# Optimization experiments

Hardware: AMD Instinct MI355X
Metric: run time of the kernel (lower is better)

Reference implementation:

```python
import jax, jax.numpy as jnp
import numpy as np

B, C, H, E, K, QT = 256, 1024, 64, 64, 2, 20000

def _mlp(x, W1, b1, W2, b2):
    # GKT MLP (eval mode: dropout off; batch-norm omitted, see notes)
    return jax.nn.relu(jax.nn.relu(x @ W1 + b1) @ W2 + b2)

def setup_inputs() -> dict:
    key = jax.random.key(0)
    ks = jax.random.split(key, 30)
    s = 0.05  # weight scale to keep pre-clamp activations in a sane range
    xt = jax.random.uniform(ks[0], (B,), dtype=jnp.float32)
    qt = jax.random.randint(ks[1], (B,), 0, QT)
    ht = jax.random.normal(ks[2], (B, C, H), dtype=jnp.float32)
    # binary question->concept incidence, ~4 KCs per question, col 0 forced on
    oh = (jax.random.uniform(ks[3], (QT, C)) < 4.0 / C).astype(jnp.float32)
    oh = oh.at[:, 0].set(1.0)
    qt_kc_one_hot = jnp.concatenate([oh, jnp.zeros((1, C), jnp.float32)], axis=0)  # zero padding row
    kc_embeddings = jax.random.normal(ks[4], (C, E), dtype=jnp.float32) * 0.1
    graphs = jax.random.uniform(ks[5], (K, C, C), dtype=jnp.float32)  # graph_model output
    neigh_weight = jnp.float32(0.8)
    MI = H + E
    Ws1 = jax.random.normal(ks[6], (MI, H), jnp.float32) * s; bs1 = jnp.zeros((H,), jnp.float32)
    Ws2 = jax.random.normal(ks[7], (H, H), jnp.float32) * s;  bs2 = jnp.zeros((H,), jnp.float32)
    Wn1 = jax.random.normal(ks[8], (K, 2 * MI, H), jnp.float32) * s; bn1 = jnp.zeros((K, H), jnp.float32)
    Wn2 = jax.random.normal(ks[9], (K, H, H), jnp.float32) * s;      bn2 = jnp.zeros((K, H), jnp.float32)
    ea_w = jax.random.uniform(ks[10], (C,), dtype=jnp.float32)
    We = jax.random.normal(ks[11], (H, H), jnp.float32) * s; be = jnp.zeros((H,), jnp.float32)
    Wa = jax.random.normal(ks[12], (H, H), jnp.float32) * s; ba = jnp.zeros((H,), jnp.float32)
    W_ih = jax.random.normal(ks[13], (H, 3 * H), jnp.float32) * s; b_ih = jnp.zeros((3 * H,), jnp.float32)
    W_hh = jax.random.normal(ks[14], (H, 3 * H), jnp.float32) * s; b_hh = jnp.zeros((3 * H,), jnp.float32)
    Wp = jax.random.normal(ks[15], (H, 1), jnp.float32) * s; bp = jnp.zeros((1,), jnp.float32)
    return dict(xt=xt, qt=qt, ht=ht, qt_kc_one_hot=qt_kc_one_hot, kc_embeddings=kc_embeddings,
                graphs=graphs, neigh_weight=neigh_weight, Ws1=Ws1, bs1=bs1, Ws2=Ws2, bs2=bs2,
                Wn1=Wn1, bn1=bn1, Wn2=Wn2, bn2=bn2, ea_w=ea_w, We=We, be=be, Wa=Wa, ba=ba,
                W_ih=W_ih, b_ih=b_ih, W_hh=W_hh, b_hh=b_hh, Wp=Wp, bp=bp)

def reference(xt, qt, ht, qt_kc_one_hot, kc_embeddings, graphs, neigh_weight,
              Ws1, bs1, Ws2, bs2, Wn1, bn1, Wn2, bn2, ea_w, We, be, Wa, ba,
              W_ih, b_ih, W_hh, b_hh, Wp, bp):
    # ---- _aggregate: the fusion loops never write back, so tmp_ht = cat(ht, kc_emb)
    mask = qt_kc_one_hot[qt]                                   # [B, C] gather of binary incidence
    kc = jnp.broadcast_to(kc_embeddings[None], (mask.shape[0], C, E))
    tmp_ht = jnp.concatenate([ht, kc], axis=-1)                # [B, C, H+E]
    # ---- _agg_neighbors
    self_ht = tmp_ht * mask[..., None]
    self_feat = jnp.clip(_mlp(self_ht, Ws1, bs1, Ws2, bs2), -10.0, 10.0)
    neigh_ht = jnp.clip(jnp.concatenate([self_ht, tmp_ht], axis=-1), -5.0, 5.0)  # [B,C,2(H+E)]
    # bug-faithful adj: mean of graphs[k] rows over sample 0's active concepts
    a0 = mask[0]                                               # [C]
    denom = jnp.maximum(a0.sum(), 1.0)
    adj = jnp.clip(jnp.einsum('c,kcd->kd', a0, graphs) / denom, -5.0, 5.0)       # [K, C]
    nb = jax.vmap(lambda W1, b1, W2, b2: _mlp(neigh_ht, W1, b1, W2, b2))(Wn1, bn1, Wn2, bn2)
    nb = jnp.clip(nb, -5.0, 5.0)                               # [K, B, C, H]
    w = jnp.clip(neigh_weight, 0.1, 0.9)
    nf = jnp.clip(adj[0][None, :, None] * nb[0], -5.0, 5.0)
    for k in range(1, K):
        nf = jnp.clip(w * nf + (1.0 - w) * adj[k][None, :, None] * nb[k], -5.0, 5.0)
    m_next = jnp.clip(jnp.where(mask[..., None] > 0.5, self_feat, nf), -50.0, 50.0)
    # ---- erase-add gate
    g = ea_w[None, :, None]
    res = m_next - g * jax.nn.sigmoid(m_next @ We + be) * m_next + g * jnp.tanh(m_next @ Wa + ba)
    # ---- GRUCell over flattened (B*C) rows
    gi = res @ W_ih + b_ih
    gh = ht @ W_hh + b_hh
    ir, iz, in_ = jnp.split(gi, 3, axis=-1)
    hr, hz, hn = jnp.split(gh, 3, axis=-1)
    r = jax.nn.sigmoid(ir + hr)
    z = jax.nn.sigmoid(iz + hz)
    n = jnp.tanh(in_ + r * hn)
    h_next = (1.0 - z) * n + z * ht                            # [B, C, H]
    y = jax.nn.sigmoid(h_next @ Wp + bp)[..., 0]               # [B, C]
    return y
```

## Files before the change

### kernel.cpp

```cpp
#include <hip/hip_runtime.h>

#define DEVINL __device__ __forceinline__

typedef __bf16 bf16x8 __attribute__((ext_vector_type(8)));
typedef float  f32x4  __attribute__((ext_vector_type(4)));
typedef unsigned u32x2 __attribute__((ext_vector_type(2)));

static constexpr size_t kAdjOff  = 0;
static constexpr size_t kBiasOff = 8192;
static constexpr size_t kFragOff = 8192 + 786432;

static constexpr int FB_Wn1h0 = 0,  FB_Wn1h1 = 8,  FB_Wn2_0 = 16, FB_Wn2_1 = 24;
static constexpr int FB_Ws1h  = 32, FB_Ws2   = 40, FB_We    = 48, FB_Wa    = 56;
static constexpr int FB_Wih   = 64, FB_Whh   = 88;

DEVINL unsigned short bf16r(float f) {
  unsigned u = __builtin_bit_cast(unsigned, f);
  unsigned r = ((u >> 16) & 1u) + 0x7FFFu;
  return (unsigned short)((u + r) >> 16);
}
DEVINL float sigmoidf_(float x) { return __builtin_amdgcn_rcpf(1.f + __expf(-x)); }
DEVINL float tanhf_(float x)    { return 1.f - 2.f * __builtin_amdgcn_rcpf(1.f + __expf(2.f * x)); }

DEVINL unsigned pkbf(float a, float b) {
  unsigned d;
  asm("v_cvt_pk_bf16_f32 %0, %1, %2" : "=v"(d) : "v"(a), "v"(b));
  return d;
}

DEVINL f32x4 mfma16(bf16x8 a, bf16x8 b, f32x4 c) {
  return __builtin_amdgcn_mfma_f32_16x16x32_bf16(a, b, c, 0, 0, 0);
}

DEVINL unsigned clip2_(unsigned x) {
  float lo = __builtin_bit_cast(float, x << 16);
  float hi = __builtin_bit_cast(float, x & 0xFFFF0000u);
  lo = fminf(fmaxf(lo, -5.f), 5.f);
  hi = fminf(fmaxf(hi, -5.f), 5.f);
  return (__builtin_bit_cast(unsigned, lo) >> 16) | (__builtin_bit_cast(unsigned, hi) & 0xFFFF0000u);
}
DEVINL bf16x8 clip5(bf16x8 a) {
  uint4 u = __builtin_bit_cast(uint4, a);
  u.x = clip2_(u.x); u.y = clip2_(u.y); u.z = clip2_(u.z); u.w = clip2_(u.w);
  return __builtin_bit_cast(bf16x8, u);
}

DEVINL void dsw64(unsigned addr, unsigned long long d) {
  asm volatile("ds_write_b64 %0, %1" :: "v"(addr), "v"(d));
}
DEVINL void ldA2_tr(unsigned addr, bf16x8& a0, bf16x8& a1) {
  u32x2 r0, r1, r2, r3;
  asm volatile(
      "ds_read_b64_tr_b16 %0, %4\n\t"
      "ds_read_b64_tr_b16 %1, %4 offset:512\n\t"
      "ds_read_b64_tr_b16 %2, %4 offset:1024\n\t"
      "ds_read_b64_tr_b16 %3, %4 offset:1536\n\t"
      "s_waitcnt lgkmcnt(0)"
      : "=&v"(r0), "=&v"(r1), "=&v"(r2), "=&v"(r3)
      : "v"(addr));
  uint4 u0{r0.x, r0.y, r1.x, r1.y};
  uint4 u1{r2.x, r2.y, r3.x, r3.y};
  a0 = __builtin_bit_cast(bf16x8, u0);
  a1 = __builtin_bit_cast(bf16x8, u1);
}

__global__ void prep_adj_kernel(const int* __restrict__ qt, const float* __restrict__ onehot,
                                const float* __restrict__ graphs, float* __restrict__ adjw) {
  __shared__ float a0v[1024];
  __shared__ int   aidx[1024];
  __shared__ int   s_nnz;
  __shared__ float s_den;
  const int tid = threadIdx.x;
  const int k = blockIdx.x >> 2, chunk = blockIdx.x & 3;
  if (tid == 0) { s_nnz = 0; s_den = 0.f; }
  __syncthreads();
  const int q0 = qt[0];
  float lsum = 0.f;
#pragma unroll
  for (int i = 0; i < 4; i++) {
    int c = tid * 4 + i;
    float v = onehot[(size_t)q0 * 1024 + c];
    lsum += v;
    if (v != 0.f) { int p = atomicAdd(&s_nnz, 1); aidx[p] = c; a0v[p] = v; }
  }
#pragma unroll
  for (int off = 32; off >= 1; off >>= 1) lsum += __shfl_xor(lsum, off, 64);
  if ((tid & 63) == 0) atomicAdd(&s_den, lsum);
  __syncthreads();
  const float denom = fmaxf(s_den, 1.f);
  const int nnz = s_nnz;
  const int d = chunk * 256 + tid;
  const float* G = graphs + (size_t)k * 1048576 + d;
  float sum = 0.f;
  for (int j = 0; j < nnz; j++) sum += a0v[j] * G[(size_t)aidx[j] * 1024];
  adjw[k * 1024 + d] = fminf(fmaxf(sum / denom, -5.f), 5.f);
}

__global__ void prep_bias_kernel(const float* __restrict__ kc, const float* __restrict__ Wn1,
                                 const float* __restrict__ bn1, const float* __restrict__ Ws1,
                                 const float* __restrict__ bs1, float* __restrict__ biasTab) {
  int gid = blockIdx.x * 256 + threadIdx.x;
  int j = gid & 63;
  int c = (gid >> 6) & 1023;
  int tab = gid >> 16;
  const float* kcr = kc + (size_t)c * 64;
  float s;
  if (tab < 2) {
    s = bn1[tab * 64 + j];
    const float* W = Wn1 + ((size_t)tab * 256 + 192) * 64 + j;
#pragma unroll 4
    for (int e = 0; e < 64; e++) s += fminf(fmaxf(kcr[e], -5.f), 5.f) * W[(size_t)e * 64];
  } else {
    s = bs1[j];
    const float* W = Ws1 + (size_t)64 * 64 + j;
#pragma unroll 4
    for (int e = 0; e < 64; e++) s += kcr[e] * W[(size_t)e * 64];
  }
  int c16 = c >> 4, rr = c & 3, qq = (c & 15) >> 2, nt = j >> 4;
  int lane = qq * 16 + (j & 15);
  biasTab[(size_t)((((c16 * 3 + tab) * 4 + nt) * 64 + lane)) * 4 + rr] = s;
}

__global__ void prep_wfrag_kernel(const float* __restrict__ Wn1, const float* __restrict__ Wn2,
                                  const float* __restrict__ Ws1, const float* __restrict__ Ws2,
                                  const float* __restrict__ We,  const float* __restrict__ Wa,
                                  const float* __restrict__ Wih, const float* __restrict__ Whh,
                                  uint4* __restrict__ wfrag) {
  const int bid = blockIdx.x, lane = threadIdx.x;
  int mat, ks, nt;
  if (bid < 64) { mat = bid >> 3; ks = (bid >> 2) & 1; nt = bid & 3; }
  else { int f2 = bid - 64; mat = 8 + f2 / 24; int f = f2 % 24; ks = f / 12; nt = f % 12; }
  const float* base = Wn1; int stride = 64;
  switch (mat) {
    case 0: base = Wn1 + (size_t)128 * 64; break;
    case 1: base = Wn1 + (size_t)(256 + 128) * 64; break;
    case 2: base = Wn2; break;
    case 3: base = Wn2 + (size_t)64 * 64; break;
    case 4: base = Ws1; break;
    case 5: base = Ws2; break;
    case 6: base = We; break;
    case 7: base = Wa; break;
    case 8: base = Wih; stride = 192; break;
    case 9: base = Whh; stride = 192; break;
  }
  const int qq = lane >> 4, col = nt * 16 + (lane & 15);
  union { unsigned short u[8]; uint4 v; } tmp;
#pragma unroll
  for (int jj = 0; jj < 8; jj++) {
    int k = ks * 32 + ((jj < 4) ? (qq * 4 + jj) : (16 + qq * 4 + (jj - 4)));
    tmp.u[jj] = bf16r(base[(size_t)k * stride + col]);
  }
  wfrag[(size_t)bid * 64 + lane] = tmp.v;
}

__global__ __launch_bounds__(256, 3) void gkt_main_kernel(
    const int* __restrict__ qt, const float* __restrict__ onehot, const float* __restrict__ ht,
    const float* __restrict__ nw, const float* __restrict__ bn2, const float* __restrict__ be,
    const float* __restrict__ ba, const float* __restrict__ bih, const float* __restrict__ bhh,
    const float* __restrict__ Wp, const float* __restrict__ bp, const float* __restrict__ eaw,
    const float* __restrict__ bs2, const float* __restrict__ adjw, const float* __restrict__ biasTab,
    const bf16x8* __restrict__ wfrag, float* __restrict__ out) {
  __shared__ __align__(128) unsigned short hbuf[4][64][16];
  __shared__ __align__(16) float tokp[4][64];
  __shared__ __align__(16) uint4 gfrag[40 * 64];

  const int tid = threadIdx.x;
  const int wv = tid >> 6, lane = tid & 63;
  const int q = lane >> 4, cl = lane & 15;
  const int t0 = (blockIdx.x * 4 + wv) * 16;
  const int b = t0 >> 10, c0 = t0 & 1023, c16 = c0 >> 4;

  unsigned short* hb = &hbuf[wv][0][0];
  float* tp = &tokp[wv][0];
  const unsigned hbA = (unsigned)(size_t)hb + lane * 8;

  {
    const uint4* wf4 = (const uint4*)wfrag;
#pragma unroll
    for (int i = 0; i < 10; i++) {
      int f = wv * 10 + i;
      gfrag[f * 64 + lane] = wf4[(64 + f) * 64 + lane];
    }
  }

  if (lane < 16) {
    const int c = c0 + lane;
    tp[lane]      = onehot[(size_t)qt[b] * 1024 + c];
    tp[16 + lane] = adjw[c];
    tp[32 + lane] = adjw[1024 + c];
    tp[48 + lane] = eaw[c];
  }
  {
    const float4* ht4 = (const float4*)ht;
#pragma unroll
    for (int i = 0; i < 4; i++) {
      float4 v = ht4[(size_t)t0 * 16 + i * 64 + lane];
      int e = i * 64 + lane;
      int tok = e >> 4, fb = (e & 15) * 4;
      hbuf[wv][fb + 0][tok] = bf16r(v.x);
      hbuf[wv][fb + 1][tok] = bf16r(v.y);
      hbuf[wv][fb + 2][tok] = bf16r(v.z);
      hbuf[wv][fb + 3][tok] = bf16r(v.w);
    }
  }

  const f32x4* bt4 = (const f32x4*)biasTab;
  f32x4 btN0[4], btN1[4], btS[4];
#pragma unroll
  for (int nt = 0; nt < 4; nt++) {
    btN0[nt] = bt4[((c16 * 3 + 0) * 4 + nt) * 64 + lane];
    btN1[nt] = bt4[((c16 * 3 + 1) * 4 + nt) * 64 + lane];
    btS[nt]  = bt4[((c16 * 3 + 2) * 4 + nt) * 64 + lane];
  }

  __syncthreads();

  const float wmix = fminf(fmaxf(nw[0], 0.1f), 0.9f);

  auto ldB = [&](int frag) -> bf16x8 { return wfrag[frag * 64 + lane]; };
  auto ldG = [&](int fr) -> bf16x8 {
    return (fr < 40) ? *(const bf16x8*)&gfrag[fr * 64 + lane]
                     : wfrag[(64 + fr) * 64 + lane];
  };
  auto ldTP4 = [&](int base) -> f32x4 {
    return *(const f32x4*)(tp + base + q * 4);
  };
  auto packRow = [&](int nt, float v0, float v1, float v2, float v3) {
    unsigned long long d = (unsigned long long)pkbf(v0, v1) |
                           ((unsigned long long)pkbf(v2, v3) << 32);
    dsw64((unsigned)(size_t)&hbuf[wv][nt * 16 + cl][q * 4], d);
  };

  bf16x8 xr[2];
  ldA2_tr(hbA, xr[0], xr[1]);

  f32x4 nf[4];
  {
    bf16x8 xc[2];
#pragma unroll
    for (int ks = 0; ks < 2; ks++) xc[ks] = clip5(xr[ks]);

#pragma unroll
    for (int k2 = 0; k2 < 2; k2++) {
      f32x4 acc[4];
#pragma unroll
      for (int nt = 0; nt < 4; nt++)
        acc[nt] = k2 ? btN1[nt] : btN0[nt];
#pragma unroll
      for (int ks = 0; ks < 2; ks++)
#pragma unroll
        for (int nt = 0; nt < 4; nt++) {
          bf16x8 bb = ldB((k2 ? FB_Wn1h1 : FB_Wn1h0) + ks * 4 + nt);
          acc[nt] = mfma16(xc[ks], bb, acc[nt]);
        }
#pragma unroll
      for (int nt = 0; nt < 4; nt++)
        packRow(nt, fmaxf(acc[nt][0], 0.f), fmaxf(acc[nt][1], 0.f),
                    fmaxf(acc[nt][2], 0.f), fmaxf(acc[nt][3], 0.f));
      bf16x8 a0, a1;
      ldA2_tr(hbA, a0, a1);
      f32x4 acc2[4];
#pragma unroll
      for (int nt = 0; nt < 4; nt++) {
        float bz = bn2[k2 * 64 + nt * 16 + cl];
        acc2[nt] = {bz, bz, bz, bz};
      }
#pragma unroll
      for (int nt = 0; nt < 4; nt++) {
        acc2[nt] = mfma16(a0, ldB((k2 ? FB_Wn2_1 : FB_Wn2_0) + nt), acc2[nt]);
        acc2[nt] = mfma16(a1, ldB((k2 ? FB_Wn2_1 : FB_Wn2_0) + 4 + nt), acc2[nt]);
      }
      {
        f32x4 adjv = ldTP4((1 + k2) * 16);
#pragma unroll
        for (int nt = 0; nt < 4; nt++)
#pragma unroll
          for (int r = 0; r < 4; r++) {
            float nb = fminf(fmaxf(acc2[nt][r], 0.f), 5.f);
            float v = adjv[r] * nb;
            if (k2 == 0) nf[nt][r] = wmix * fminf(fmaxf(v, -5.f), 5.f);
            else         nf[nt][r] = fminf(fmaxf(nf[nt][r] + (1.f - wmix) * v, -5.f), 5.f);
          }
      }
    }
  }

  bool anySelf = __any((lane < 16) && (tp[lane] > 0.5f));
  if (anySelf) {
    f32x4 acc[4];
#pragma unroll
    for (int nt = 0; nt < 4; nt++) acc[nt] = btS[nt];
#pragma unroll
    for (int ks = 0; ks < 2; ks++)
#pragma unroll
      for (int nt = 0; nt < 4; nt++) {
        bf16x8 bb = ldB(FB_Ws1h + ks * 4 + nt);
        acc[nt] = mfma16(xr[ks], bb, acc[nt]);
      }
#pragma unroll
    for (int nt = 0; nt < 4; nt++)
      packRow(nt, fmaxf(acc[nt][0], 0.f), fmaxf(acc[nt][1], 0.f),
                  fmaxf(acc[nt][2], 0.f), fmaxf(acc[nt][3], 0.f));
    bf16x8 a0, a1;
    ldA2_tr(hbA, a0, a1);
    f32x4 acc2[4];
#pragma unroll
    for (int nt = 0; nt < 4; nt++) {
      float bz = bs2[nt * 16 + cl];
      acc2[nt] = {bz, bz, bz, bz};
    }
#pragma unroll
    for (int nt = 0; nt < 4; nt++) {
      acc2[nt] = mfma16(a0, ldB(FB_Ws2 + nt), acc2[nt]);
      acc2[nt] = mfma16(a1, ldB(FB_Ws2 + 4 + nt), acc2[nt]);
    }
    {
      f32x4 mk = ldTP4(0);
#pragma unroll
      for (int nt = 0; nt < 4; nt++)
#pragma unroll
        for (int r = 0; r < 4; r++) {
          float sf = fminf(fmaxf(acc2[nt][r], 0.f), 10.f);
          nf[nt][r] = (mk[r] > 0.5f) ? sf : nf[nt][r];
        }
    }
  }

#pragma unroll
  for (int nt = 0; nt < 4; nt++)
    packRow(nt, nf[nt][0], nf[nt][1], nf[nt][2], nf[nt][3]);
  bf16x8 mf[2];
  ldA2_tr(hbA, mf[0], mf[1]);
  {
    f32x4 accE[4];
#pragma unroll
    for (int nt = 0; nt < 4; nt++) {
      float bz = be[nt * 16 + cl];
      accE[nt] = {bz, bz, bz, bz};
    }
#pragma unroll
    for (int ks = 0; ks < 2; ks++)
#pragma unroll
      for (int nt = 0; nt < 4; nt++) {
        bf16x8 bb = ldB(FB_We + ks * 4 + nt);
        accE[nt] = mfma16(mf[ks], bb, accE[nt]);
      }
    {
      f32x4 gv = ldTP4(48);
#pragma unroll
      for (int nt = 0; nt < 4; nt++)
#pragma unroll
        for (int r = 0; r < 4; r++) {
          float m = nf[nt][r];
          nf[nt][r] = m - gv[r] * sigmoidf_(accE[nt][r]) * m;
        }
    }
    f32x4 accA[4];
#pragma unroll
    for (int nt = 0; nt < 4; nt++) {
      float bz = ba[nt * 16 + cl];
      accA[nt] = {bz, bz, bz, bz};
    }
#pragma unroll
    for (int ks = 0; ks < 2; ks++)
#pragma unroll
      for (int nt = 0; nt < 4; nt++) {
        bf16x8 bb = ldB(FB_Wa + ks * 4 + nt);
        accA[nt] = mfma16(mf[ks], bb, accA[nt]);
      }
    {
      f32x4 gv = ldTP4(48);
#pragma unroll
      for (int nt = 0; nt < 4; nt++)
#pragma unroll
        for (int r = 0; r < 4; r++)
          nf[nt][r] += gv[r] * tanhf_(accA[nt][r]);
    }
  }

#pragma unroll
  for (int nt = 0; nt < 4; nt++)
    packRow(nt, nf[nt][0], nf[nt][1], nf[nt][2], nf[nt][3]);
  bf16x8 rf[2];
  ldA2_tr(hbA, rf[0], rf[1]);

  f32x4 gR[4], gZ[4], gN[4], gH[4];
#pragma unroll
  for (int nt = 0; nt < 4; nt++) {
    int col = nt * 16 + cl;
    float brz = bih[col] + bhh[col];
    float bzz = bih[64 + col] + bhh[64 + col];
    float bnn = bih[128 + col];
    float bhn = bhh[128 + col];
    gR[nt] = {brz, brz, brz, brz};
    gZ[nt] = {bzz, bzz, bzz, bzz};
    gN[nt] = {bnn, bnn, bnn, bnn};
    gH[nt] = {bhn, bhn, bhn, bhn};
  }
#pragma unroll
  for (int ks = 0; ks < 2; ks++)
#pragma unroll
    for (int nt = 0; nt < 4; nt++) {
      bf16x8 bi_r = ldG(ks * 12 + nt);
      bf16x8 bh_r = ldG(24 + ks * 12 + nt);
      bf16x8 bi_z = ldG(ks * 12 + 4 + nt);
      bf16x8 bh_z = ldG(24 + ks * 12 + 4 + nt);
      bf16x8 bi_n = ldG(ks * 12 + 8 + nt);
      bf16x8 bh_n = ldG(24 + ks * 12 + 8 + nt);
      gR[nt] = mfma16(rf[ks], bi_r, gR[nt]);
      gR[nt] = mfma16(xr[ks], bh_r, gR[nt]);
      gZ[nt] = mfma16(rf[ks], bi_z, gZ[nt]);
      gZ[nt] = mfma16(xr[ks], bh_z, gZ[nt]);
      gN[nt] = mfma16(rf[ks], bi_n, gN[nt]);
      gH[nt] = mfma16(xr[ks], bh_n, gH[nt]);
    }

  float wp4[4];
#pragma unroll
  for (int nt = 0; nt < 4; nt++) wp4[nt] = Wp[nt * 16 + cl];
  const float bpv = bp[0];

#pragma unroll
  for (int r = 0; r < 4; r++) {
    int tok = q * 4 + r;
    float part = 0.f;
#pragma unroll
    for (int nt = 0; nt < 4; nt++) {
      float rr = sigmoidf_(gR[nt][r]);
      float zz = sigmoidf_(gZ[nt][r]);
      float nval = tanhf_(gN[nt][r] + rr * gH[nt][r]);
      float htv = ht[(size_t)(t0 + tok) * 64 + nt * 16 + cl];
      float hnx = (1.f - zz) * nval + zz * htv;
      part += hnx * wp4[nt];
    }
    part += __shfl_xor(part, 1, 64);
    part += __shfl_xor(part, 2, 64);
    part += __shfl_xor(part, 4, 64);
    part += __shfl_xor(part, 8, 64);
    if (cl == 0) out[t0 + tok] = sigmoidf_(part + bpv);
  }
}

extern "C" void kernel_launch(void* const* d_in, const int* in_sizes, int n_in,
                              void* d_out, int out_size, void* d_ws, size_t ws_size,
                              hipStream_t stream) {
  const int*   qt     = (const int*)d_in[1];
  const float* ht     = (const float*)d_in[2];
  const float* onehot = (const float*)d_in[3];
  const float* kc     = (const float*)d_in[4];
  const float* graphs = (const float*)d_in[5];
  const float* nw     = (const float*)d_in[6];
  const float* Ws1    = (const float*)d_in[7];
  const float* bs1    = (const float*)d_in[8];
  const float* Ws2    = (const float*)d_in[9];
  const float* bs2    = (const float*)d_in[10];
  const float* Wn1    = (const float*)d_in[11];
  const float* bn1    = (const float*)d_in[12];
  const float* Wn2    = (const float*)d_in[13];
  const float* bn2    = (const float*)d_in[14];
  const float* eaw    = (const float*)d_in[15];
  const float* We     = (const float*)d_in[16];
  const float* be     = (const float*)d_in[17];
  const float* Wa     = (const float*)d_in[18];
  const float* ba     = (const float*)d_in[19];
  const float* Wih    = (const float*)d_in[20];
  const float* bih    = (const float*)d_in[21];
  const float* Whh    = (const float*)d_in[22];
  const float* bhh    = (const float*)d_in[23];
  const float* Wp     = (const float*)d_in[24];
  const float* bp     = (const float*)d_in[25];
  float* out = (float*)d_out;

  float* adjw    = (float*)((char*)d_ws + kAdjOff);
  float* biasTab = (float*)((char*)d_ws + kBiasOff);
  uint4* wfragU  = (uint4*)((char*)d_ws + kFragOff);

  prep_adj_kernel<<<8, 256, 0, stream>>>(qt, onehot, graphs, adjw);
  prep_bias_kernel<<<768, 256, 0, stream>>>(kc, Wn1, bn1, Ws1, bs1, biasTab);
  prep_wfrag_kernel<<<112, 64, 0, stream>>>(Wn1, Wn2, Ws1, Ws2, We, Wa, Wih, Whh, wfragU);
  gkt_main_kernel<<<4096, 256, 0, stream>>>(qt, onehot, ht, nw, bn2, be, ba, bih, bhh,
                                            Wp, bp, eaw, bs2, adjw, biasTab,
                                            (const bf16x8*)wfragU, out);
}
```

Baseline: 276.0 us.

## Process two 16-token tiles per wave to reuse weight fragments in registers

Each wave now handles 32 tokens as two 16-token sub-tiles (A/B) that share weight fragments loaded once into registers (fX/fY), rather than reloading them from global memory for every MFMA. The grid is halved and launch bounds drop from 3 to 2 blocks per SIMD to leave room for the larger register footprint. The aim is to cut repeated global and L2 weight-fragment traffic and give more independent MFMAs to interleave. The cost is lower occupancy and higher register pressure, which may limit latency hiding.

Result: faster. 266.6 us (-3.4%).

```diff
diff --git a/kernel.cpp b/kernel.cpp
--- a/kernel.cpp
+++ b/kernel.cpp
@@ -153,26 +153,29 @@
   wfrag[(size_t)bid * 64 + lane] = tmp.v;
 }
 
-__global__ __launch_bounds__(256, 3) void gkt_main_kernel(
+__global__ __launch_bounds__(256, 2) void gkt_main_kernel(
     const int* __restrict__ qt, const float* __restrict__ onehot, const float* __restrict__ ht,
     const float* __restrict__ nw, const float* __restrict__ bn2, const float* __restrict__ be,
     const float* __restrict__ ba, const float* __restrict__ bih, const float* __restrict__ bhh,
     const float* __restrict__ Wp, const float* __restrict__ bp, const float* __restrict__ eaw,
     const float* __restrict__ bs2, const float* __restrict__ adjw, const float* __restrict__ biasTab,
     const bf16x8* __restrict__ wfrag, float* __restrict__ out) {
-  __shared__ __align__(128) unsigned short hbuf[4][64][16];
-  __shared__ __align__(16) float tokp[4][64];
+  __shared__ __align__(128) unsigned short hbuf[4][2][64][16];
+  __shared__ __align__(16) float tokp[4][2][64];
   __shared__ __align__(16) uint4 gfrag[40 * 64];
 
   const int tid = threadIdx.x;
   const int wv = tid >> 6, lane = tid & 63;
   const int q = lane >> 4, cl = lane & 15;
-  const int t0 = (blockIdx.x * 4 + wv) * 16;
+  const int t0 = (blockIdx.x * 4 + wv) * 32;
   const int b = t0 >> 10, c0 = t0 & 1023, c16 = c0 >> 4;
 
-  unsigned short* hb = &hbuf[wv][0][0];
-  float* tp = &tokp[wv][0];
-  const unsigned hbA = (unsigned)(size_t)hb + lane * 8;
+  const unsigned hbA = (unsigned)(size_t)&hbuf[wv][0][0][0] + lane * 8;
+  const unsigned hbB = hbA + 2048;
+  const unsigned pbA = (unsigned)(size_t)&hbuf[wv][0][0][0] + cl * 32 + q * 8;
+  const unsigned pbB = pbA + 2048;
+  float* tpA = &tokp[wv][0][0];
+  float* tpB = &tokp[wv][1][0];
 
   {
     const uint4* wf4 = (const uint4*)wfrag;
@@ -183,208 +186,261 @@
     }
   }
 
-  if (lane < 16) {
+  if (lane < 32) {
+    const int s = lane >> 4, l = lane & 15;
     const int c = c0 + lane;
-    tp[lane]      = onehot[(size_t)qt[b] * 1024 + c];
-    tp[16 + lane] = adjw[c];
-    tp[32 + lane] = adjw[1024 + c];
-    tp[48 + lane] = eaw[c];
+    float* tp = &tokp[wv][s][0];
+    tp[l]      = onehot[(size_t)qt[b] * 1024 + c];
+    tp[16 + l] = adjw[c];
+    tp[32 + l] = adjw[1024 + c];
+    tp[48 + l] = eaw[c];
   }
   {
     const float4* ht4 = (const float4*)ht;
 #pragma unroll
-    for (int i = 0; i < 4; i++) {
+    for (int i = 0; i < 8; i++) {
       float4 v = ht4[(size_t)t0 * 16 + i * 64 + lane];
       int e = i * 64 + lane;
-      int tok = e >> 4, fb = (e & 15) * 4;
-      hbuf[wv][fb + 0][tok] = bf16r(v.x);
-      hbuf[wv][fb + 1][tok] = bf16r(v.y);
-      hbuf[wv][fb + 2][tok] = bf16r(v.z);
-      hbuf[wv][fb + 3][tok] = bf16r(v.w);
-    }
-  }
-
-  const f32x4* bt4 = (const f32x4*)biasTab;
-  f32x4 btN0[4], btN1[4], btS[4];
-#pragma unroll
-  for (int nt = 0; nt < 4; nt++) {
-    btN0[nt] = bt4[((c16 * 3 + 0) * 4 + nt) * 64 + lane];
-    btN1[nt] = bt4[((c16 * 3 + 1) * 4 + nt) * 64 + lane];
-    btS[nt]  = bt4[((c16 * 3 + 2) * 4 + nt) * 64 + lane];
-  }
-
-  __syncthreads();
-
-  const float wmix = fminf(fmaxf(nw[0], 0.1f), 0.9f);
+      int tok = e >> 4, s = tok >> 4, tk = tok & 15, fb = (e & 15) * 4;
+      hbuf[wv][s][fb + 0][tk] = bf16r(v.x);
+      hbuf[wv][s][fb + 1][tk] = bf16r(v.y);
+      hbuf[wv][s][fb + 2][tk] = bf16r(v.z);
+      hbuf[wv][s][fb + 3][tk] = bf16r(v.w);
+    }
+  }
 
   auto ldB = [&](int frag) -> bf16x8 { return wfrag[frag * 64 + lane]; };
   auto ldG = [&](int fr) -> bf16x8 {
     return (fr < 40) ? *(const bf16x8*)&gfrag[fr * 64 + lane]
                      : wfrag[(64 + fr) * 64 + lane];
   };
-  auto ldTP4 = [&](int base) -> f32x4 {
+  auto ldTP4 = [&](const float* tp, int base) -> f32x4 {
     return *(const f32x4*)(tp + base + q * 4);
   };
-  auto packRow = [&](int nt, float v0, float v1, float v2, float v3) {
+  auto packRow = [&](unsigned pb, int nt, float v0, float v1, float v2, float v3) {
     unsigned long long d = (unsigned long long)pkbf(v0, v1) |
                            ((unsigned long long)pkbf(v2, v3) << 32);
-    dsw64((unsigned)(size_t)&hbuf[wv][nt * 16 + cl][q * 4], d);
+    dsw64(pb + nt * 512, d);
   };
-
-  bf16x8 xr[2];
-  ldA2_tr(hbA, xr[0], xr[1]);
-
-  f32x4 nf[4];
+  const f32x4* bt4 = (const f32x4*)biasTab;
+
+  bf16x8 fX[8], fY[8];
+#pragma unroll
+  for (int i = 0; i < 8; i++) fX[i] = ldB(FB_Wn1h0 + i);
+
+  __syncthreads();
+
+  const float wmix = fminf(fmaxf(nw[0], 0.1f), 0.9f);
+
+  bf16x8 xrA[2], xrB[2];
+  ldA2_tr(hbA, xrA[0], xrA[1]);
+  ldA2_tr(hbB, xrB[0], xrB[1]);
+  bf16x8 xcA[2], xcB[2];
+#pragma unroll
+  for (int ks = 0; ks < 2; ks++) { xcA[ks] = clip5(xrA[ks]); xcB[ks] = clip5(xrB[ks]); }
+
+  f32x4 nfA[4], nfB[4];
+
+#pragma unroll
+  for (int k2 = 0; k2 < 2; k2++) {
+#pragma unroll
+    for (int i = 0; i < 8; i++) fY[i] = ldB((k2 ? FB_Wn2_1 : FB_Wn2_0) + i);
+    f32x4 acA[4], acB[4];
+#pragma unroll
+    for (int nt = 0; nt < 4; nt++) {
+      acA[nt] = bt4[((c16 * 3 + k2) * 4 + nt) * 64 + lane];
+      acB[nt] = bt4[(((c16 + 1) * 3 + k2) * 4 + nt) * 64 + lane];
+    }
+#pragma unroll
+    for (int ks = 0; ks < 2; ks++)
+#pragma unroll
+      for (int nt = 0; nt < 4; nt++) {
+        acA[nt] = mfma16(xcA[ks], fX[ks * 4 + nt], acA[nt]);
+        acB[nt] = mfma16(xcB[ks], fX[ks * 4 + nt], acB[nt]);
+      }
+#pragma unroll
+    for (int nt = 0; nt < 4; nt++)
+      packRow(pbA, nt, fmaxf(acA[nt][0], 0.f), fmaxf(acA[nt][1], 0.f),
+                       fmaxf(acA[nt][2], 0.f), fmaxf(acA[nt][3], 0.f));
+#pragma unroll
+    for (int nt = 0; nt < 4; nt++)
+      packRow(pbB, nt, fmaxf(acB[nt][0], 0.f), fmaxf(acB[nt][1], 0.f),
+                       fmaxf(acB[nt][2], 0.f), fmaxf(acB[nt][3], 0.f));
+
+#pragma unroll
+    for (int i = 0; i < 8; i++) fX[i] = ldB((k2 ? FB_Ws1h : FB_Wn1h1) + i);
+    bf16x8 a0, a1;
+    f32x4 c2A[4], c2B[4];
+#pragma unroll
+    for (int nt = 0; nt < 4; nt++) {
+      float bz = bn2[k2 * 64 + nt * 16 + cl];
+      c2A[nt] = {bz, bz, bz, bz};
+      c2B[nt] = c2A[nt];
+    }
+    ldA2_tr(hbA, a0, a1);
+#pragma unroll
+    for (int nt = 0; nt < 4; nt++) {
+      c2A[nt] = mfma16(a0, fY[nt], c2A[nt]);
+      c2A[nt] = mfma16(a1, fY[4 + nt], c2A[nt]);
+    }
+    ldA2_tr(hbB, a0, a1);
+#pragma unroll
+    for (int nt = 0; nt < 4; nt++) {
+      c2B[nt] = mfma16(a0, fY[nt], c2B[nt]);
+      c2B[nt] = mfma16(a1, fY[4 + nt], c2B[nt]);
+    }
+    {
+      f32x4 avA = ldTP4(tpA, (1 + k2) * 16), avB = ldTP4(tpB, (1 + k2) * 16);
+#pragma unroll
+      for (int nt = 0; nt < 4; nt++)
+#pragma unroll
+        for (int r = 0; r < 4; r++) {
+          float nbA = fminf(fmaxf(c2A[nt][r], 0.f), 5.f);
+          float nbB = fminf(fmaxf(c2B[nt][r], 0.f), 5.f);
+          float vA = avA[r] * nbA, vB = avB[r] * nbB;
+          if (k2 == 0) {
+            nfA[nt][r] = wmix * fminf(fmaxf(vA, -5.f), 5.f);
+            nfB[nt][r] = wmix * fminf(fmaxf(vB, -5.f), 5.f);
+          } else {
+            nfA[nt][r] = fminf(fmaxf(nfA[nt][r] + (1.f - wmix) * vA, -5.f), 5.f);
+            nfB[nt][r] = fminf(fmaxf(nfB[nt][r] + (1.f - wmix) * vB, -5.f), 5.f);
+          }
+        }
+    }
+  }
+
+  bool anySelf = __any((lane < 32) && (tokp[wv][lane >> 4][lane & 15] > 0.5f));
+  if (anySelf) {
+#pragma unroll
+    for (int i = 0; i < 8; i++) fY[i] = ldB(FB_Ws2 + i);
+    f32x4 acA[4], acB[4];
+#pragma unroll
+    for (int nt = 0; nt < 4; nt++) {
+      acA[nt] = bt4[((c16 * 3 + 2) * 4 + nt) * 64 + lane];
+      acB[nt] = bt4[(((c16 + 1) * 3 + 2) * 4 + nt) * 64 + lane];
+    }
+#pragma unroll
+    for (int ks = 0; ks < 2; ks++)
+#pragma unroll
+      for (int nt = 0; nt < 4; nt++) {
+        acA[nt] = mfma16(xrA[ks], fX[ks * 4 + nt], acA[nt]);
+        acB[nt] = mfma16(xrB[ks], fX[ks * 4 + nt], acB[nt]);
+      }
+#pragma unroll
+    for (int nt = 0; nt < 4; nt++)
+      packRow(pbA, nt, fmaxf(acA[nt][0], 0.f), fmaxf(acA[nt][1], 0.f),
+                       fmaxf(acA[nt][2], 0.f), fmaxf(acA[nt][3], 0.f));
+#pragma unroll
+    for (int nt = 0; nt < 4; nt++)
+      packRow(pbB, nt, fmaxf(acB[nt][0], 0.f), fmaxf(acB[nt][1], 0.f),
+                       fmaxf(acB[nt][2], 0.f), fmaxf(acB[nt][3], 0.f));
+    bf16x8 a0, a1;
+    f32x4 c2A[4], c2B[4];
+#pragma unroll
+    for (int nt = 0; nt < 4; nt++) {
+      float bz = bs2[nt * 16 + cl];
+      c2A[nt] = {bz, bz, bz, bz};
+      c2B[nt] = c2A[nt];
+    }
+    ldA2_tr(hbA, a0, a1);
+#pragma unroll
+    for (int nt = 0; nt < 4; nt++) {
+      c2A[nt] = mfma16(a0, fY[nt], c2A[nt]);
+      c2A[nt] = mfma16(a1, fY[4 + nt], c2A[nt]);
+    }
+    ldA2_tr(hbB, a0, a1);
+#pragma unroll
+    for (int nt = 0; nt < 4; nt++) {
+      c2B[nt] = mfma16(a0, fY[nt], c2B[nt]);
+      c2B[nt] = mfma16(a1, fY[4 + nt], c2B[nt]);
+    }
+    {
+      f32x4 mkA = ldTP4(tpA, 0), mkB = ldTP4(tpB, 0);
+#pragma unroll
+      for (int nt = 0; nt < 4; nt++)
+#pragma unroll
+        for (int r = 0; r < 4; r++) {
+          float sfA = fminf(fmaxf(c2A[nt][r], 0.f), 10.f);
+          float sfB = fminf(fmaxf(c2B[nt][r], 0.f), 10.f);
+          nfA[nt][r] = (mkA[r] > 0.5f) ? sfA : nfA[nt][r];
+          nfB[nt][r] = (mkB[r] > 0.5f) ? sfB : nfB[nt][r];
+        }
+    }
+  }
+
+#pragma unroll
+  for (int i = 0; i < 8; i++) fX[i] = ldB(FB_We + i);
+#pragma unroll
+  for (int nt = 0; nt < 4; nt++) packRow(pbA, nt, nfA[nt][0], nfA[nt][1], nfA[nt][2], nfA[nt][3]);
+#pragma unroll
+  for (int nt = 0; nt < 4; nt++) packRow(pbB, nt, nfB[nt][0], nfB[nt][1], nfB[nt][2], nfB[nt][3]);
+  bf16x8 mfA[2], mfB[2];
+  ldA2_tr(hbA, mfA[0], mfA[1]);
+  ldA2_tr(hbB, mfB[0], mfB[1]);
   {
-    bf16x8 xc[2];
-#pragma unroll
-    for (int ks = 0; ks < 2; ks++) xc[ks] = clip5(xr[ks]);
-
-#pragma unroll
-    for (int k2 = 0; k2 < 2; k2++) {
-      f32x4 acc[4];
-#pragma unroll
-      for (int nt = 0; nt < 4; nt++)
-        acc[nt] = k2 ? btN1[nt] : btN0[nt];
-#pragma unroll
-      for (int ks = 0; ks < 2; ks++)
-#pragma unroll
-        for (int nt = 0; nt < 4; nt++) {
-          bf16x8 bb = ldB((k2 ? FB_Wn1h1 : FB_Wn1h0) + ks * 4 + nt);
-          acc[nt] = mfma16(xc[ks], bb, acc[nt]);
-        }
-#pragma unroll
-      for (int nt = 0; nt < 4; nt++)
-        packRow(nt, fmaxf(acc[nt][0], 0.f), fmaxf(acc[nt][1], 0.f),
-                    fmaxf(acc[nt][2], 0.f), fmaxf(acc[nt][3], 0.f));
-      bf16x8 a0, a1;
-      ldA2_tr(hbA, a0, a1);
-      f32x4 acc2[4];
+#pragma unroll
+    for (int i = 0; i < 8; i++) fY[i] = ldB(FB_Wa + i);
+    f32x4 eA[4], eB[4];
+#pragma unroll
+    for (int nt = 0; nt < 4; nt++) {
+      float bz = be[nt * 16 + cl];
+      eA[nt] = {bz, bz, bz, bz};
+      eB[nt] = eA[nt];
+    }
+#pragma unroll
+    for (int ks = 0; ks < 2; ks++)
 #pragma unroll
       for (int nt = 0; nt < 4; nt++) {
-        float bz = bn2[k2 * 64 + nt * 16 + cl];
-        acc2[nt] = {bz, bz, bz, bz};
-      }
-#pragma unroll
-      for (int nt = 0; nt < 4; nt++) {
-        acc2[nt] = mfma16(a0, ldB((k2 ? FB_Wn2_1 : FB_Wn2_0) + nt), acc2[nt]);
-        acc2[nt] = mfma16(a1, ldB((k2 ? FB_Wn2_1 : FB_Wn2_0) + 4 + nt), acc2[nt]);
-      }
-      {
-        f32x4 adjv = ldTP4((1 + k2) * 16);
-#pragma unroll
-        for (int nt = 0; nt < 4; nt++)
-#pragma unroll
-          for (int r = 0; r < 4; r++) {
-            float nb = fminf(fmaxf(acc2[nt][r], 0.f), 5.f);
-            float v = adjv[r] * nb;
-            if (k2 == 0) nf[nt][r] = wmix * fminf(fmaxf(v, -5.f), 5.f);
-            else         nf[nt][r] = fminf(fmaxf(nf[nt][r] + (1.f - wmix) * v, -5.f), 5.f);
-          }
-      }
-    }
-  }
-
-  bool anySelf = __any((lane < 16) && (tp[lane] > 0.5f));
-  if (anySelf) {
-    f32x4 acc[4];
-#pragma unroll
-    for (int nt = 0; nt < 4; nt++) acc[nt] = btS[nt];
-#pragma unroll
-    for (int ks = 0; ks < 2; ks++)
-#pragma unroll
-      for (int nt = 0; nt < 4; nt++) {
-        bf16x8 bb = ldB(FB_Ws1h + ks * 4 + nt);
-        acc[nt] = mfma16(xr[ks], bb, acc[nt]);
-      }
-#pragma unroll
-    for (int nt = 0; nt < 4; nt++)
-      packRow(nt, fmaxf(acc[nt][0], 0.f), fmaxf(acc[nt][1], 0.f),
-                  fmaxf(acc[nt][2], 0.f), fmaxf(acc[nt][3], 0.f));
-    bf16x8 a0, a1;
-    ldA2_tr(hbA, a0, a1);
-    f32x4 acc2[4];
-#pragma unroll
-    for (int nt = 0; nt < 4; nt++) {
-      float bz = bs2[nt * 16 + cl];
-      acc2[nt] = {bz, bz, bz, bz};
-    }
-#pragma unroll
-    for (int nt = 0; nt < 4; nt++) {
-      acc2[nt] = mfma16(a0, ldB(FB_Ws2 + nt), acc2[nt]);
-      acc2[nt] = mfma16(a1, ldB(FB_Ws2 + 4 + nt), acc2[nt]);
-    }
-    {
-      f32x4 mk = ldTP4(0);
-#pragma unroll
-      for (int nt = 0; nt < 4; nt++)
-#pragma unroll
-        for (int r = 0; r < 4; r++) {
-          float sf = fminf(fmaxf(acc2[nt][r], 0.f), 10.f);
-          nf[nt][r] = (mk[r] > 0.5f) ? sf : nf[nt][r];
-        }
-    }
-  }
-
-#pragma unroll
-  for (int nt = 0; nt < 4; nt++)
-    packRow(nt, nf[nt][0], nf[nt][1], nf[nt][2], nf[nt][3]);
-  bf16x8 mf[2];
-  ldA2_tr(hbA, mf[0], mf[1]);
-  {
-    f32x4 accE[4];
-#pragma unroll
-    for (int nt = 0; nt < 4; nt++) {
-      float bz = be[nt * 16 + cl];
-      accE[nt] = {bz, bz, bz, bz};
-    }
-#pragma unroll
-    for (int ks = 0; ks < 2; ks++)
-#pragma unroll
-      for (int nt = 0; nt < 4; nt++) {
-        bf16x8 bb = ldB(FB_We + ks * 4 + nt);
-        accE[nt] = mfma16(mf[ks], bb, accE[nt]);
+        eA[nt] = mfma16(mfA[ks], fX[ks * 4 + nt], eA[nt]);
+        eB[nt] = mfma16(mfB[ks], fX[ks * 4 + nt], eB[nt]);
       }
     {
-      f32x4 gv = ldTP4(48);
+      f32x4 gvA = ldTP4(tpA, 48), gvB = ldTP4(tpB, 48);
 #pragma unroll
       for (int nt = 0; nt < 4; nt++)
 #pragma unroll
         for (int r = 0; r < 4; r++) {
-          float m = nf[nt][r];
-          nf[nt][r] = m - gv[r] * sigmoidf_(accE[nt][r]) * m;
+          float mA = nfA[nt][r], mB = nfB[nt][r];
+          nfA[nt][r] = mA - gvA[r] * sigmoidf_(eA[nt][r]) * mA;
+          nfB[nt][r] = mB - gvB[r] * sigmoidf_(eB[nt][r]) * mB;
         }
     }
-    f32x4 accA[4];
+    f32x4 aA[4], aB[4];
 #pragma unroll
     for (int nt = 0; nt < 4; nt++) {
       float bz = ba[nt * 16 + cl];
-      accA[nt] = {bz, bz, bz, bz};
+      aA[nt] = {bz, bz, bz, bz};
+      aB[nt] = aA[nt];
     }
 #pragma unroll
     for (int ks = 0; ks < 2; ks++)
 #pragma unroll
       for (int nt = 0; nt < 4; nt++) {
-        bf16x8 bb = ldB(FB_Wa + ks * 4 + nt);
-        accA[nt] = mfma16(mf[ks], bb, accA[nt]);
+        aA[nt] = mfma16(mfA[ks], fY[ks * 4 + nt], aA[nt]);
+        aB[nt] = mfma16(mfB[ks], fY[ks * 4 + nt], aB[nt]);
       }
     {
-      f32x4 gv = ldTP4(48);
+      f32x4 gvA = ldTP4(tpA, 48), gvB = ldTP4(tpB, 48);
 #pragma unroll
       for (int nt = 0; nt < 4; nt++)
 #pragma unroll
-        for (int r = 0; r < 4; r++)
-          nf[nt][r] += gv[r] * tanhf_(accA[nt][r]);
-    }
-  }
-
-#pragma unroll
-  for (int nt = 0; nt < 4; nt++)
-    packRow(nt, nf[nt][0], nf[nt][1], nf[nt][2], nf[nt][3]);
-  bf16x8 rf[2];
-  ldA2_tr(hbA, rf[0], rf[1]);
-
-  f32x4 gR[4], gZ[4], gN[4], gH[4];
+        for (int r = 0; r < 4; r++) {
+          nfA[nt][r] += gvA[r] * tanhf_(aA[nt][r]);
+          nfB[nt][r] += gvB[r] * tanhf_(aB[nt][r]);
+        }
+    }
+  }
+
+#pragma unroll
+  for (int nt = 0; nt < 4; nt++) packRow(pbA, nt, nfA[nt][0], nfA[nt][1], nfA[nt][2], nfA[nt][3]);
+#pragma unroll
+  for (int nt = 0; nt < 4; nt++) packRow(pbB, nt, nfB[nt][0], nfB[nt][1], nfB[nt][2], nfB[nt][3]);
+  bf16x8 rfA[2], rfB[2];
+  ldA2_tr(hbA, rfA[0], rfA[1]);
+  ldA2_tr(hbB, rfB[0], rfB[1]);
+
+  f32x4 gRA[4], gZA[4], gNA[4], gHA[4];
+  f32x4 gRB[4], gZB[4], gNB[4], gHB[4];
 #pragma unroll
   for (int nt = 0; nt < 4; nt++) {
     int col = nt * 16 + cl;
@@ -392,10 +448,11 @@
     float bzz = bih[64 + col] + bhh[64 + col];
     float bnn = bih[128 + col];
     float bhn = bhh[128 + col];
-    gR[nt] = {brz, brz, brz, brz};
-    gZ[nt] = {bzz, bzz, bzz, bzz};
-    gN[nt] = {bnn, bnn, bnn, bnn};
-    gH[nt] = {bhn, bhn, bhn, bhn};
+    f32x4 v;
+    v = {brz, brz, brz, brz}; gRA[nt] = v; gRB[nt] = v;
+    v = {bzz, bzz, bzz, bzz}; gZA[nt] = v; gZB[nt] = v;
+    v = {bnn, bnn, bnn, bnn}; gNA[nt] = v; gNB[nt] = v;
+    v = {bhn, bhn, bhn, bhn}; gHA[nt] = v; gHB[nt] = v;
   }
 #pragma unroll
   for (int ks = 0; ks < 2; ks++)
@@ -407,12 +464,18 @@
       bf16x8 bh_z = ldG(24 + ks * 12 + 4 + nt);
       bf16x8 bi_n = ldG(ks * 12 + 8 + nt);
       bf16x8 bh_n = ldG(24 + ks * 12 + 8 + nt);
-      gR[nt] = mfma16(rf[ks], bi_r, gR[nt]);
-      gR[nt] = mfma16(xr[ks], bh_r, gR[nt]);
-      gZ[nt] = mfma16(rf[ks], bi_z, gZ[nt]);
-      gZ[nt] = mfma16(xr[ks], bh_z, gZ[nt]);
-      gN[nt] = mfma16(rf[ks], bi_n, gN[nt]);
-      gH[nt] = mfma16(xr[ks], bh_n, gH[nt]);
+      gRA[nt] = mfma16(rfA[ks], bi_r, gRA[nt]);
+      gRA[nt] = mfma16(xrA[ks], bh_r, gRA[nt]);
+      gZA[nt] = mfma16(rfA[ks], bi_z, gZA[nt]);
+      gZA[nt] = mfma16(xrA[ks], bh_z, gZA[nt]);
+      gNA[nt] = mfma16(rfA[ks], bi_n, gNA[nt]);
+      gHA[nt] = mfma16(xrA[ks], bh_n, gHA[nt]);
+      gRB[nt] = mfma16(rfB[ks], bi_r, gRB[nt]);
+      gRB[nt] = mfma16(xrB[ks], bh_r, gRB[nt]);
+      gZB[nt] = mfma16(rfB[ks], bi_z, gZB[nt]);
+      gZB[nt] = mfma16(xrB[ks], bh_z, gZB[nt]);
+      gNB[nt] = mfma16(rfB[ks], bi_n, gNB[nt]);
+      gHB[nt] = mfma16(xrB[ks], bh_n, gHB[nt]);
     }
 
   float wp4[4];
@@ -426,9 +489,28 @@
     float part = 0.f;
 #pragma unroll
     for (int nt = 0; nt < 4; nt++) {
-      float rr = sigmoidf_(gR[nt][r]);
-      float zz = sigmoidf_(gZ[nt][r]);
-      float nval = tanhf_(gN[nt][r] + rr * gH[nt][r]);
+      float rr = sigmoidf_(gRA[nt][r]);
+      float zz = sigmoidf_(gZA[nt][r]);
+      float nval = tanhf_(gNA[nt][r] + rr * gHA[nt][r]);
+      float htv = ht[(size_t)(t0 + tok) * 64 + nt * 16 + cl];
+      float hnx = (1.f - zz) * nval + zz * htv;
+      part += hnx * wp4[nt];
+    }
+    part += __shfl_xor(part, 1, 64);
+    part += __shfl_xor(part, 2, 64);
+    part += __shfl_xor(part, 4, 64);
+    part += __shfl_xor(part, 8, 64);
+    if (cl == 0) out[t0 + tok] = sigmoidf_(part + bpv);
+  }
+#pragma unroll
+  for (int r = 0; r < 4; r++) {
+    int tok = 16 + q * 4 + r;
+    float part = 0.f;
+#pragma unroll
+    for (int nt = 0; nt < 4; nt++) {
+      float rr = sigmoidf_(gRB[nt][r]);
+      float zz = sigmoidf_(gZB[nt][r]);
+      float nval = tanhf_(gNB[nt][r] + rr * gHB[nt][r]);
       float htv = ht[(size_t)(t0 + tok) * 64 + nt * 16 + cl];
       float hnx = (1.f - zz) * nval + zz * htv;
       part += hnx * wp4[nt];
@@ -478,7 +560,7 @@
   prep_adj_kernel<<<8, 256, 0, stream>>>(qt, onehot, graphs, adjw);
   prep_bias_kernel<<<768, 256, 0, stream>>>(kc, Wn1, bn1, Ws1, bs1, biasTab);
   prep_wfrag_kernel<<<112, 64, 0, stream>>>(Wn1, Wn2, Ws1, Ws2, We, Wa, Wih, Whh, wfragU);
-  gkt_main_kernel<<<4096, 256, 0, stream>>>(qt, onehot, ht, nw, bn2, be, ba, bih, bhh,
+  gkt_main_kernel<<<2048, 256, 0, stream>>>(qt, onehot, ht, nw, bn2, be, ba, bih, bhh,
                                             Wp, bp, eaw, bs2, adjw, biasTab,
                                             (const bf16x8*)wfragU, out);
 }
```
